# Kernel tuning notes

Hardware: AMD Instinct MI355X
Metric: run time of the kernel (lower is better)

The kernel has to match this reference:

```python
import jax, jax.numpy as jnp
import numpy as np

D = 1024
H = 16
HD = D // H  # 64
FF = 4 * D
EPS = 1e-5

def _layernorm(x, g, b):
    mu = jnp.mean(x, axis=-1, keepdims=True)
    var = jnp.mean((x - mu) ** 2, axis=-1, keepdims=True)
    return (x - mu) * jax.lax.rsqrt(var + EPS) * g + b

def _apply_rotary(x, cos, sin):
    # x: [B,H,T,HD]; cos/sin: [T,HD//2] broadcast over B,H
    d = x.shape[-1] // 2
    x1, x2 = x[..., :d], x[..., d:]
    return jnp.concatenate([x1 * cos - x2 * sin, x2 * cos + x1 * sin], axis=-1)

def setup_inputs() -> dict:
    key = jax.random.key(0)
    ks = jax.random.split(key, 12)
    B, T = 4, 2048
    s = 0.02
    return {
        "x": jax.random.normal(ks[0], (B, T, D), jnp.float32),
        "rope_cos": jax.random.uniform(ks[1], (T, HD // 2), jnp.float32),
        "rope_sin": jax.random.uniform(ks[2], (T, HD // 2), jnp.float32),
        "ln1_g": jnp.ones((D,), jnp.float32),
        "ln1_b": jnp.zeros((D,), jnp.float32),
        "Wqkv": jax.random.normal(ks[3], (D, 3 * D), jnp.float32) * s,
        "bqkv": jnp.zeros((3 * D,), jnp.float32),
        "Wo": jax.random.normal(ks[4], (D, D), jnp.float32) * s,
        "bo": jnp.zeros((D,), jnp.float32),
        "ln2_g": jnp.ones((D,), jnp.float32),
        "ln2_b": jnp.zeros((D,), jnp.float32),
        "W1": jax.random.normal(ks[5], (D, FF), jnp.float32) * s,
        "b1": jnp.zeros((FF,), jnp.float32),
        "W2": jax.random.normal(ks[6], (FF, D), jnp.float32) * s,
        "b2": jnp.zeros((D,), jnp.float32),
    }

def reference(x, rope_cos, rope_sin, ln1_g, ln1_b, Wqkv, bqkv, Wo, bo, ln2_g, ln2_b, W1, b1, W2, b2):
    B, T, _ = x.shape
    h = _layernorm(x, ln1_g, ln1_b)
    qkv = (h @ Wqkv + bqkv).reshape(B, T, 3, H, HD)
    qkv = jnp.transpose(qkv, (2, 0, 3, 1, 4))  # [3,B,H,T,HD]
    q, k, v = qkv[0], qkv[1], qkv[2]
    q = _apply_rotary(q, rope_cos, rope_sin)
    k = _apply_rotary(k, rope_cos, rope_sin)
    scale = 1.0 / jnp.sqrt(jnp.float32(HD))
    scores = jnp.einsum('bhqd,bhkd->bhqk', q, k) * scale
    probs = jax.nn.softmax(scores, axis=-1)
    attn = jnp.einsum('bhqk,bhkd->bhqd', probs, v)
    attn = jnp.transpose(attn, (0, 2, 1, 3)).reshape(B, T, D)
    x = x + attn @ Wo + bo
    h2 = _layernorm(x, ln2_g, ln2_b)
    mlp = jax.nn.gelu(h2 @ W1 + b1, approximate=False) @ W2 + b2
    return x + mlp
```

## Files before the change

### kernel.cpp

```cpp
#include <hip/hip_runtime.h>
#include <hip/hip_bf16.h>
#include <math.h>

typedef __bf16 bf16x8 __attribute__((ext_vector_type(8)));
typedef float f32x4 __attribute__((ext_vector_type(4)));
typedef float f32x16 __attribute__((ext_vector_type(16)));
typedef unsigned short u16x8 __attribute__((ext_vector_type(8)));
typedef unsigned short u16x4 __attribute__((ext_vector_type(4)));
typedef unsigned int u32x4 __attribute__((ext_vector_type(4)));

#define DEV __device__ __forceinline__

DEV unsigned short f2bf(float f) { __bf16 h = (__bf16)f; return __builtin_bit_cast(unsigned short, h); }
DEV float bf2f(unsigned short u) { __bf16 h = __builtin_bit_cast(__bf16, u); return (float)h; }
DEV unsigned int pk2(float a, float b) {
  return (unsigned int)f2bf(a) | ((unsigned int)f2bf(b) << 16);
}

DEV void async_cp16(const void* g, void* l) {
  __builtin_amdgcn_global_load_lds((const __attribute__((address_space(1))) void*)g,
                                   (__attribute__((address_space(3))) void*)l, 16, 0, 0);
}

#define PHASE_BAR()  do { __builtin_amdgcn_s_barrier(); __builtin_amdgcn_sched_barrier(0); } while (0)
#define WAIT_LGKM0() do { asm volatile("s_waitcnt lgkmcnt(0)" ::: "memory"); __builtin_amdgcn_sched_barrier(0); } while (0)
#define WAIT_VM(n)   do { asm volatile("s_waitcnt vmcnt(" #n ")" ::: "memory"); __builtin_amdgcn_sched_barrier(0); } while (0)

__global__ __launch_bounds__(256) void ln_kernel(const float* __restrict__ in,
    const float* __restrict__ g, const float* __restrict__ b,
    unsigned short* __restrict__ out)
{
  const int row = blockIdx.x;
  const int tid = threadIdx.x;
  const float4 v = ((const float4*)(in + (size_t)row * 1024))[tid];
  float s  = v.x + v.y + v.z + v.w;
  float sq = v.x*v.x + v.y*v.y + v.z*v.z + v.w*v.w;
  for (int m = 1; m < 64; m <<= 1) { s += __shfl_xor(s, m); sq += __shfl_xor(sq, m); }
  __shared__ float red[8];
  const int wave = tid >> 6;
  if ((tid & 63) == 0) { red[wave] = s; red[4 + wave] = sq; }
  __syncthreads();
  s  = red[0] + red[1] + red[2] + red[3];
  sq = red[4] + red[5] + red[6] + red[7];
  const float mu = s * (1.0f / 1024.0f);
  const float var = sq * (1.0f / 1024.0f) - mu * mu;
  const float rs = rsqrtf(var + 1e-5f);
  const float4 gv = ((const float4*)g)[tid];
  const float4 bv = ((const float4*)b)[tid];
  u16x4 o;
  o[0] = f2bf((v.x - mu) * rs * gv.x + bv.x);
  o[1] = f2bf((v.y - mu) * rs * gv.y + bv.y);
  o[2] = f2bf((v.z - mu) * rs * gv.z + bv.z);
  o[3] = f2bf((v.w - mu) * rs * gv.w + bv.w);
  *(u16x4*)(out + (size_t)row * 1024 + tid * 4) = o;
}

__global__ __launch_bounds__(256) void wtrans_kernel(const float* __restrict__ in,
    unsigned short* __restrict__ out, int K, int N)
{
  __shared__ float tile[32][33];
  const int n0 = blockIdx.x * 32, k0 = blockIdx.y * 32;
  const int r = threadIdx.x >> 5, c = threadIdx.x & 31;
  for (int p = 0; p < 4; ++p)
    tile[r + p * 8][c] = in[(size_t)(k0 + r + p * 8) * N + n0 + c];
  __syncthreads();
  for (int p = 0; p < 4; ++p)
    out[(size_t)(n0 + r + p * 8) * K + k0 + c] = f2bf(tile[c][r + p * 8]);
}

enum { EPI_QKV = 0, EPI_ATTNO = 1, EPI_GELU = 2, EPI_FINAL = 3 };

template <int EPI>
__global__ __launch_bounds__(256, 3) void gemm_bt(
    const unsigned short* __restrict__ A,
    const unsigned short* __restrict__ Bt,
    const float* __restrict__ bias,
    const float* __restrict__ resid,
    void* __restrict__ out,
    int M, int N, int K,
    const float* __restrict__ rc, const float* __restrict__ rsn,
    unsigned short* __restrict__ vout)
{
  __shared__ unsigned short lA[8192] __attribute__((aligned(16)));
  __shared__ unsigned short lB[8192] __attribute__((aligned(16)));
  const int tid = threadIdx.x;
  const int lane = tid & 63, wave = tid >> 6;
  const int l15 = lane & 15, quad = lane >> 4;
  const int bm = blockIdx.x * 128, bn = blockIdx.y * 128;
  const int wm = (wave & 1) * 64, wn = (wave >> 1) * 64;

  const unsigned short* ga[4]; const unsigned short* gb[4];
  unsigned short* la_dst[4]; unsigned short* lb_dst[4];
  for (int it = 0; it < 4; ++it) {
    const int s = it * 256 + tid;
    const int row = s >> 3;
    const int ch = (s & 7) ^ (row & 7);
    ga[it] = A  + (size_t)(bm + row) * K + ch * 8;
    gb[it] = Bt + (size_t)(bn + row) * K + ch * 8;
    const int base = (it * 256 + wave * 64) * 8;
    la_dst[it] = lA + base;
    lb_dst[it] = lB + base;
  }
  int offA[2][4], offB[2][4];
  for (int ks = 0; ks < 2; ++ks)
    for (int i = 0; i < 4; ++i) {
      int row = wm + i * 16 + l15;
      offA[ks][i] = (row * 8 + ((ks * 4 + quad) ^ (row & 7))) * 8;
      row = wn + i * 16 + l15;
      offB[ks][i] = (row * 8 + ((ks * 4 + quad) ^ (row & 7))) * 8;
    }

  f32x4 acc[4][4];
  for (int i = 0; i < 4; ++i)
    for (int j = 0; j < 4; ++j)
      acc[i][j] = f32x4{0.f, 0.f, 0.f, 0.f};

  for (int k0 = 0; k0 < K; k0 += 64) {
    for (int it = 0; it < 4; ++it) async_cp16(ga[it], la_dst[it]);
    for (int it = 0; it < 4; ++it) async_cp16(gb[it], lb_dst[it]);
    for (int it = 0; it < 4; ++it) { ga[it] += 64; gb[it] += 64; }
    __syncthreads();
    for (int ks = 0; ks < 2; ++ks) {
      bf16x8 af[4], bfr[4];
      for (int i = 0; i < 4; ++i) af[i]  = *(const bf16x8*)(lA + offA[ks][i]);
      for (int j = 0; j < 4; ++j) bfr[j] = *(const bf16x8*)(lB + offB[ks][j]);
      for (int i = 0; i < 4; ++i)
        for (int j = 0; j < 4; ++j)
          acc[i][j] = __builtin_amdgcn_mfma_f32_16x16x32_bf16(af[i], bfr[j], acc[i][j], 0, 0, 0);
    }
    __syncthreads();
  }

  float bvals[4];
  for (int j = 0; j < 4; ++j) bvals[j] = bias[bn + wn + j * 16 + l15];

  for (int i = 0; i < 4; ++i) {
    for (int r = 0; r < 4; ++r) {
      const size_t row = bm + wm + i * 16 + quad * 4 + r;
      for (int j = 0; j < 4; ++j) {
        const size_t col = bn + wn + j * 16 + l15;
        const float v = acc[i][j][r] + bvals[j];
        const size_t idx = row * (size_t)N + col;
        if constexpr (EPI == EPI_ATTNO) {
          ((float*)out)[idx] = resid[idx] + v;
        } else if constexpr (EPI == EPI_GELU) {
          const float gl = 0.5f * v * (1.0f + erff(v * 0.70710678118f));
          ((unsigned short*)out)[idx] = f2bf(gl);
        } else {
          ((float*)out)[idx] = resid[idx] + v;
        }
      }
    }
  }
}

template <int EPI>
__global__ __launch_bounds__(512, 1) void gemm256(
    const unsigned short* __restrict__ A,
    const unsigned short* __restrict__ Bt,
    const float* __restrict__ bias,
    void* __restrict__ out,
    int M, int N, int K,
    const float* __restrict__ rc, const float* __restrict__ rsn,
    unsigned short* __restrict__ vout)
{
  __shared__ unsigned short lA[2][16384] __attribute__((aligned(16)));
  __shared__ unsigned short lB[2][16384] __attribute__((aligned(16)));
  const int tid = threadIdx.x;
  const int lane = tid & 63, wave = tid >> 6;
  const int l15 = lane & 15, quad = lane >> 4;
  const int bm = blockIdx.x * 256, bn = blockIdx.y * 256;
  const int wr = wave >> 2, wc = wave & 3;
  const int wm = wr * 128, wn = wc * 64;

  const unsigned short* gA[4]; const unsigned short* gB[4];
  {
    const int r0 = tid >> 3;
    const int ch = (tid & 7) ^ (r0 & 7);
    for (int it = 0; it < 4; ++it) {
      gA[it] = A  + (size_t)(bm + it * 64 + r0) * K + ch * 8;
      gB[it] = Bt + (size_t)(bn + it * 64 + r0) * K + ch * 8;
    }
  }
  const int ldsbase = wave * 512;

  const int swz = l15 & 7;
  const int oA0 = (wm + l15) * 64 + ((quad) ^ swz) * 8;
  const int oA1 = (wm + l15) * 64 + ((4 + quad) ^ swz) * 8;
  const int oB0 = (wn + l15) * 64 + ((quad) ^ swz) * 8;
  const int oB1 = (wn + l15) * 64 + ((4 + quad) ^ swz) * 8;

  f32x4 acc[8][4];
  for (int i = 0; i < 8; ++i)
    for (int j = 0; j < 4; ++j)
      acc[i][j] = f32x4{0.f, 0.f, 0.f, 0.f};

  const int NT = K >> 6;

  async_cp16(gB[0], lB[0] + 0    + ldsbase);
  async_cp16(gB[1], lB[0] + 4096 + ldsbase);
  async_cp16(gB[2], lB[0] + 8192 + ldsbase);
  async_cp16(gB[3], lB[0] + 12288 + ldsbase);
  async_cp16(gA[0], lA[0] + 0    + ldsbase);
  async_cp16(gA[2], lA[0] + 8192 + ldsbase);
  async_cp16(gA[1], lA[0] + 4096 + ldsbase);
  async_cp16(gA[3], lA[0] + 12288 + ldsbase);
  for (int it = 0; it < 4; ++it) { gA[it] += 64; gB[it] += 64; }
  WAIT_VM(2);
  PHASE_BAR();

  for (int t = 0; t < NT; ++t) {
    const unsigned short* lAc = lA[t & 1];
    const unsigned short* lBc = lB[t & 1];
    unsigned short* lAn = lA[(t & 1) ^ 1];
    unsigned short* lBn = lB[(t & 1) ^ 1];
    const bool pf = (t + 1 < NT);
    bf16x8 af[4], bfr[4];

    for (int i = 0; i < 4; ++i) af[i]  = *(const bf16x8*)(lAc + oA0 + i * 1024);
    for (int j = 0; j < 4; ++j) bfr[j] = *(const bf16x8*)(lBc + oB0 + j * 1024);
    if (pf) { async_cp16(gB[0], lBn + 0 + ldsbase); async_cp16(gB[1], lBn + 4096 + ldsbase); }
    PHASE_BAR(); WAIT_LGKM0();
    __builtin_amdgcn_s_setprio(1);
    for (int i = 0; i < 4; ++i)
      for (int j = 0; j < 4; ++j)
        acc[i][j] = __builtin_amdgcn_mfma_f32_16x16x32_bf16(af[i], bfr[j], acc[i][j], 0, 0, 0);
    __builtin_amdgcn_s_setprio(0);
    if (pf) { WAIT_VM(2); } else { WAIT_VM(0); }
    PHASE_BAR();

    for (int i = 0; i < 4; ++i) af[i] = *(const bf16x8*)(lAc + oA0 + (4 + i) * 1024);
    if (pf) { async_cp16(gB[2], lBn + 8192 + ldsbase); async_cp16(gB[3], lBn + 12288 + ldsbase); }
    PHASE_BAR(); WAIT_LGKM0();
    __builtin_amdgcn_s_setprio(1);
    for (int i = 0; i < 4; ++i)
      for (int j = 0; j < 4; ++j)
        acc[4 + i][j] = __builtin_amdgcn_mfma_f32_16x16x32_bf16(af[i], bfr[j], acc[4 + i][j], 0, 0, 0);
    __builtin_amdgcn_s_setprio(0);
    PHASE_BAR();

    for (int i = 0; i < 4; ++i) af[i]  = *(const bf16x8*)(lAc + oA1 + i * 1024);
    for (int j = 0; j < 4; ++j) bfr[j] = *(const bf16x8*)(lBc + oB1 + j * 1024);
    if (pf) { async_cp16(gA[0], lAn + 0 + ldsbase); async_cp16(gA[2], lAn + 8192 + ldsbase); }
    PHASE_BAR(); WAIT_LGKM0();
    __builtin_amdgcn_s_setprio(1);
    for (int i = 0; i < 4; ++i)
      for (int j = 0; j < 4; ++j)
        acc[i][j] = __builtin_amdgcn_mfma_f32_16x16x32_bf16(af[i], bfr[j], acc[i][j], 0, 0, 0);
    __builtin_amdgcn_s_setprio(0);
    PHASE_BAR();

    for (int i = 0; i < 4; ++i) af[i] = *(const bf16x8*)(lAc + oA1 + (4 + i) * 1024);
    if (pf) { async_cp16(gA[1], lAn + 4096 + ldsbase); async_cp16(gA[3], lAn + 12288 + ldsbase); }
    PHASE_BAR(); WAIT_LGKM0();
    __builtin_amdgcn_s_setprio(1);
    for (int i = 0; i < 4; ++i)
      for (int j = 0; j < 4; ++j)
        acc[4 + i][j] = __builtin_amdgcn_mfma_f32_16x16x32_bf16(af[i], bfr[j], acc[4 + i][j], 0, 0, 0);
    __builtin_amdgcn_s_setprio(0);
    if (pf) { WAIT_VM(2); }
    PHASE_BAR();

    if (pf) for (int it = 0; it < 4; ++it) { gA[it] += 64; gB[it] += 64; }
  }

  float bvals[4];
  for (int j = 0; j < 4; ++j) bvals[j] = bias[bn + wn + j * 16 + l15];

  if constexpr (EPI == EPI_QKV) {
    const int cn = bn + wn;
    const int sec = cn >> 10;
    if (sec == 2) {
      const int b = bm >> 11;
      const int hh = (cn & 1023) >> 6;
      for (int i = 0; i < 8; ++i) {
        const int t0 = (bm + wm + i * 16 + quad * 4) & 2047;
        for (int j = 0; j < 4; ++j) {
          const int d = j * 16 + l15;
          u16x4 o;
          for (int r = 0; r < 4; ++r) o[r] = f2bf(acc[i][j][r] + bvals[j]);
          *(u16x4*)(vout + ((size_t)((b * 16 + hh) * 64 + d)) * 2048 + t0) = o;
        }
      }
    } else {
      const float qscale = (sec == 0) ? 0.18033688f : 1.0f;
      unsigned short* qkvout = (unsigned short*)out;
      for (int i = 0; i < 8; ++i) {
        for (int r = 0; r < 4; ++r) {
          const int row = bm + wm + i * 16 + quad * 4 + r;
          const int tt = row & 2047;
          for (int j = 0; j < 2; ++j) {
            const int d = j * 16 + l15;
            const float v1 = acc[i][j][r] + bvals[j];
            const float v2 = acc[i][j + 2][r] + bvals[j + 2];
            const float c = rc[tt * 32 + d], s = rsn[tt * 32 + d];
            const float o1 = (v1 * c - v2 * s) * qscale;
            const float o2 = (v2 * c + v1 * s) * qscale;
            const size_t base = (size_t)row * 3072 + cn + d;
            qkvout[base] = f2bf(o1);
            qkvout[base + 32] = f2bf(o2);
          }
        }
      }
    }
  } else {
    unsigned short* o = (unsigned short*)out;
    for (int i = 0; i < 8; ++i)
      for (int r = 0; r < 4; ++r) {
        const size_t row = bm + wm + i * 16 + quad * 4 + r;
        for (int j = 0; j < 4; ++j) {
          const size_t col = bn + wn + j * 16 + l15;
          const float v = acc[i][j][r] + bvals[j];
          const float gl = 0.5f * v * (1.0f + erff(v * 0.70710678118f));
          o[row * (size_t)N + col] = f2bf(gl);
        }
      }
  }
}

__global__ __launch_bounds__(256, 4) void attn_kernel(
    const unsigned short* __restrict__ qkv,
    const unsigned short* __restrict__ vt,
    unsigned short* __restrict__ outb)
{
  __shared__ unsigned short Ks[2][4096] __attribute__((aligned(16)));
  __shared__ unsigned short Vs[2][4096] __attribute__((aligned(16)));
  __shared__ float Sred[128];

  const int tid = threadIdx.x;
  const int lane = tid & 63, wave = tid >> 6;
  const int l31 = lane & 31, hl = lane >> 5;
  const int bh = blockIdx.y, b = bh >> 4, h = bh & 15;
  const int q0 = blockIdx.x * 128;
  const int qsub = wave * 32;

  bf16x8 qf[4];
  {
    const unsigned short* qp = qkv + (size_t)(b * 2048 + q0 + qsub + l31) * 3072 + h * 64 + hl * 8;
    for (int kc = 0; kc < 4; ++kc) qf[kc] = *(const bf16x8*)(qp + kc * 16);
  }

  const int s0 = wave * 128 + lane, s1 = s0 + 64;
  const int r0 = s0 >> 3, c0 = (lane & 7) ^ (r0 & 7);
  const int r1 = s1 >> 3, c1 = (lane & 7) ^ (r1 & 7);
  const unsigned short* kbase = qkv + (size_t)(b * 2048) * 3072 + 1024 + h * 64;
  const unsigned short* ks0 = kbase + (size_t)r0 * 3072 + c0 * 8;
  const unsigned short* ks1 = kbase + (size_t)r1 * 3072 + c1 * 8;
  const unsigned short* vbase = vt + (size_t)bh * 64 * 2048;
  const unsigned short* vs0 = vbase + (size_t)r0 * 2048 + c0 * 8;
  const unsigned short* vs1 = vbase + (size_t)r1 * 2048 + c1 * 8;
  unsigned short* kd[2] = { Ks[0] + wave * 1024, Ks[1] + wave * 1024 };
  unsigned short* vd[2] = { Vs[0] + wave * 1024, Vs[1] + wave * 1024 };

  int offK[2][4], offV[2][4];
  for (int g = 0; g < 2; ++g)
    for (int kc = 0; kc < 4; ++kc) {
      const int rk = g * 32 + l31;
      offK[g][kc] = (rk * 8 + ((2 * kc + hl) ^ (rk & 7))) * 8;
    }
  for (int dn = 0; dn < 2; ++dn)
    for (int t = 0; t < 4; ++t) {
      const int rv = dn * 32 + l31;
      offV[dn][t] = (rv * 8 + ((2 * t + hl) ^ (rv & 7))) * 8;
    }

  f32x16 accO[2];
  for (int dn = 0; dn < 2; ++dn)
    for (int i = 0; i < 16; ++i) accO[dn][i] = 0.f;
  float rsum = 0.f;

  async_cp16(ks0, kd[0]);
  async_cp16(ks1, kd[0] + 512);
  async_cp16(vs0, vd[0]);
  async_cp16(vs1, vd[0] + 512);

  for (int kt = 0; kt < 32; ++kt) {
    const int cur = kt & 1, nxt = cur ^ 1;
    __syncthreads();
    if (kt < 31) {
      const size_t ko = (size_t)(kt + 1) * 64 * 3072;
      const int vo = (kt + 1) * 64;
      async_cp16(ks0 + ko, kd[nxt]);
      async_cp16(ks1 + ko, kd[nxt] + 512);
      async_cp16(vs0 + vo, vd[nxt]);
      async_cp16(vs1 + vo, vd[nxt] + 512);
    }
    for (int g = 0; g < 2; ++g) {
      f32x16 accS;
      for (int i = 0; i < 16; ++i) accS[i] = 0.f;
      for (int kc = 0; kc < 4; ++kc) {
        const bf16x8 kf = *(const bf16x8*)(Ks[cur] + offK[g][kc]);
        accS = __builtin_amdgcn_mfma_f32_32x32x16_bf16(kf, qf[kc], accS, 0, 0, 0);
      }
      float p[16];
      for (int i = 0; i < 16; ++i) {
        p[i] = __builtin_amdgcn_exp2f(accS[i]);
        rsum += p[i];
      }
      for (int c = 0; c < 2; ++c) {
        const unsigned int xlo0 = pk2(p[8 * c + 0], p[8 * c + 1]);
        const unsigned int xlo1 = pk2(p[8 * c + 2], p[8 * c + 3]);
        const unsigned int xhi0 = pk2(p[8 * c + 4], p[8 * c + 5]);
        const unsigned int xhi1 = pk2(p[8 * c + 6], p[8 * c + 7]);
        const auto sw0 = __builtin_amdgcn_permlane32_swap(xlo0, xhi0, false, false);
        const auto sw1 = __builtin_amdgcn_permlane32_swap(xlo1, xhi1, false, false);
        u32x4 w;
        w[0] = sw0[0];
        w[1] = sw1[0];
        w[2] = sw0[1];
        w[3] = sw1[1];
        const bf16x8 pf = __builtin_bit_cast(bf16x8, w);
        const int t = 2 * g + c;
        for (int dn = 0; dn < 2; ++dn) {
          const bf16x8 vf = *(const bf16x8*)(Vs[cur] + offV[dn][t]);
          accO[dn] = __builtin_amdgcn_mfma_f32_32x32x16_bf16(pf, vf, accO[dn], 0, 0, 0);
        }
      }
    }
  }

  {
    const float rs2 = rsum + __shfl_xor(rsum, 32);
    if (hl == 0) Sred[qsub + l31] = rs2;
  }
  __syncthreads();
  for (int reg = 0; reg < 16; ++reg) {
    const int rq = qsub + (reg & 3) + 8 * (reg >> 2) + 4 * hl;
    const float inv = 1.0f / Sred[rq];
    const size_t row = (size_t)(b * 2048 + q0 + rq);
    for (int dn = 0; dn < 2; ++dn)
      outb[row * 1024 + h * 64 + dn * 32 + l31] = f2bf(accO[dn][reg] * inv);
  }
}

extern "C" void kernel_launch(void* const* d_in, const int* in_sizes, int n_in,
                              void* d_out, int out_size, void* d_ws, size_t ws_size,
                              hipStream_t stream)
{
  const float* x        = (const float*)d_in[0];
  const float* rope_cos = (const float*)d_in[1];
  const float* rope_sin = (const float*)d_in[2];
  const float* ln1_g    = (const float*)d_in[3];
  const float* ln1_b    = (const float*)d_in[4];
  const float* Wqkv     = (const float*)d_in[5];
  const float* bqkv     = (const float*)d_in[6];
  const float* Wo       = (const float*)d_in[7];
  const float* bo       = (const float*)d_in[8];
  const float* ln2_g    = (const float*)d_in[9];
  const float* ln2_b    = (const float*)d_in[10];
  const float* W1       = (const float*)d_in[11];
  const float* b1       = (const float*)d_in[12];
  const float* W2       = (const float*)d_in[13];
  const float* b2       = (const float*)d_in[14];
  float* outp = (float*)d_out;

  char* ws = (char*)d_ws;
  size_t off = 0;
  auto alloc = [&](size_t bytes) -> void* {
    void* p = ws + off;
    off += (bytes + 255) & ~(size_t)255;
    return p;
  };
  unsigned short* h1    = (unsigned short*)alloc(8192ull * 1024 * 2);
  unsigned short* wqkvT = (unsigned short*)alloc(3072ull * 1024 * 2);
  unsigned short* woT   = (unsigned short*)alloc(1024ull * 1024 * 2);
  unsigned short* w1T   = (unsigned short*)alloc(4096ull * 1024 * 2);
  unsigned short* w2T   = (unsigned short*)alloc(1024ull * 4096 * 2);
  unsigned short* qkv   = (unsigned short*)alloc(8192ull * 3072 * 2);
  unsigned short* vtb   = (unsigned short*)alloc(64ull * 64 * 2048 * 2);
  unsigned short* h2    = (unsigned short*)alloc(8192ull * 1024 * 2);
  unsigned short* ffb   = (unsigned short*)alloc(8192ull * 4096 * 2);

  wtrans_kernel<<<dim3(96, 32), 256, 0, stream>>>(Wqkv, wqkvT, 1024, 3072);
  wtrans_kernel<<<dim3(32, 32), 256, 0, stream>>>(Wo, woT, 1024, 1024);
  wtrans_kernel<<<dim3(128, 32), 256, 0, stream>>>(W1, w1T, 1024, 4096);
  wtrans_kernel<<<dim3(32, 128), 256, 0, stream>>>(W2, w2T, 4096, 1024);

  ln_kernel<<<8192, 256, 0, stream>>>(x, ln1_g, ln1_b, h1);
  gemm256<EPI_QKV><<<dim3(32, 12), 512, 0, stream>>>(h1, wqkvT, bqkv, qkv,
                                                     8192, 3072, 1024, rope_cos, rope_sin, vtb);
  attn_kernel<<<dim3(16, 64), 256, 0, stream>>>(qkv, vtb, h1);
  gemm_bt<EPI_ATTNO><<<dim3(64, 8), 256, 0, stream>>>(h1, woT, bo, x, d_out,
                                                      8192, 1024, 1024, nullptr, nullptr, nullptr);
  ln_kernel<<<8192, 256, 0, stream>>>(outp, ln2_g, ln2_b, h2);
  gemm256<EPI_GELU><<<dim3(32, 16), 512, 0, stream>>>(h2, w1T, b1, ffb,
                                                      8192, 4096, 1024, nullptr, nullptr, nullptr);
  gemm_bt<EPI_FINAL><<<dim3(64, 8), 256, 0, stream>>>(ffb, w2T, b2, outp, d_out,
                                                      8192, 1024, 4096, nullptr, nullptr, nullptr);
}
```

Before: 605.6 us.

## Pin GEMM accumulators to AGPRs and target two waves per EU

Replaces the MFMA builtin with inline asm that keeps the accumulators in AGPRs. It also sets waves_per_eu(2,2) so two 512-thread blocks can share a CU, and recomputes global load addresses from a single lane offset instead of keeping eight pointers live. The aim is to lower VGPR pressure so occupancy can double and LDS latency is better hidden. The inline asm hides dependencies from the compiler's scheduler, which is why manual s_nops are added after the loop to cover the MFMA result hazard. The LDS use of 128KB per block may still limit residency to one block per CU.

```diff
diff --git a/kernel.cpp b/kernel.cpp
--- a/kernel.cpp
+++ b/kernel.cpp
@@ -20,6 +20,11 @@
 DEV void async_cp16(const void* g, void* l) {
   __builtin_amdgcn_global_load_lds((const __attribute__((address_space(1))) void*)g,
                                    (__attribute__((address_space(3))) void*)l, 16, 0, 0);
+}
+
+DEV void mfma_agpr(f32x4& c, bf16x8 a, bf16x8 b) {
+  asm volatile("v_mfma_f32_16x16x32_bf16 %0, %1, %2, %0"
+               : "+a"(c) : "v"(a), "v"(b));
 }
 
 #define PHASE_BAR()  do { __builtin_amdgcn_s_barrier(); __builtin_amdgcn_sched_barrier(0); } while (0)
@@ -155,7 +160,9 @@
 }
 
 template <int EPI>
-__global__ __launch_bounds__(512, 1) void gemm256(
+__global__ __launch_bounds__(512)
+__attribute__((amdgpu_waves_per_eu(2, 2)))
+void gemm256(
     const unsigned short* __restrict__ A,
     const unsigned short* __restrict__ Bt,
     const float* __restrict__ bias,
@@ -173,15 +180,9 @@
   const int wr = wave >> 2, wc = wave & 3;
   const int wm = wr * 128, wn = wc * 64;
 
-  const unsigned short* gA[4]; const unsigned short* gB[4];
-  {
-    const int r0 = tid >> 3;
-    const int ch = (tid & 7) ^ (r0 & 7);
-    for (int it = 0; it < 4; ++it) {
-      gA[it] = A  + (size_t)(bm + it * 64 + r0) * K + ch * 8;
-      gB[it] = Bt + (size_t)(bn + it * 64 + r0) * K + ch * 8;
-    }
-  }
+  const int r0 = tid >> 3;
+  const int ch = (tid & 7) ^ (r0 & 7);
+  const size_t laneOff = (size_t)r0 * K + ch * 8;
   const int ldsbase = wave * 512;
 
   const int swz = l15 & 7;
@@ -197,15 +198,16 @@
 
   const int NT = K >> 6;
 
-  async_cp16(gB[0], lB[0] + 0    + ldsbase);
-  async_cp16(gB[1], lB[0] + 4096 + ldsbase);
-  async_cp16(gB[2], lB[0] + 8192 + ldsbase);
-  async_cp16(gB[3], lB[0] + 12288 + ldsbase);
-  async_cp16(gA[0], lA[0] + 0    + ldsbase);
-  async_cp16(gA[2], lA[0] + 8192 + ldsbase);
-  async_cp16(gA[1], lA[0] + 4096 + ldsbase);
-  async_cp16(gA[3], lA[0] + 12288 + ldsbase);
-  for (int it = 0; it < 4; ++it) { gA[it] += 64; gB[it] += 64; }
+  auto stA = [&](int it, int k0, unsigned short* dst) {
+    async_cp16(A + (size_t)(bm + it * 64) * K + k0 + laneOff, dst + it * 4096 + ldsbase);
+  };
+  auto stB = [&](int it, int k0, unsigned short* dst) {
+    async_cp16(Bt + (size_t)(bn + it * 64) * K + k0 + laneOff, dst + it * 4096 + ldsbase);
+  };
+
+  stB(0, 0, lB[0]); stB(1, 0, lB[0]); stB(2, 0, lB[0]); stB(3, 0, lB[0]);
+  stA(0, 0, lA[0]); stA(2, 0, lA[0]);
+  stA(1, 0, lA[0]); stA(3, 0, lA[0]);
   WAIT_VM(2);
   PHASE_BAR();
 
@@ -215,54 +217,55 @@
     unsigned short* lAn = lA[(t & 1) ^ 1];
     unsigned short* lBn = lB[(t & 1) ^ 1];
     const bool pf = (t + 1 < NT);
+    const int kn = (t + 1) * 64;
     bf16x8 af[4], bfr[4];
 
     for (int i = 0; i < 4; ++i) af[i]  = *(const bf16x8*)(lAc + oA0 + i * 1024);
     for (int j = 0; j < 4; ++j) bfr[j] = *(const bf16x8*)(lBc + oB0 + j * 1024);
-    if (pf) { async_cp16(gB[0], lBn + 0 + ldsbase); async_cp16(gB[1], lBn + 4096 + ldsbase); }
+    if (pf) { stB(0, kn, lBn); stB(1, kn, lBn); }
     PHASE_BAR(); WAIT_LGKM0();
     __builtin_amdgcn_s_setprio(1);
     for (int i = 0; i < 4; ++i)
       for (int j = 0; j < 4; ++j)
-        acc[i][j] = __builtin_amdgcn_mfma_f32_16x16x32_bf16(af[i], bfr[j], acc[i][j], 0, 0, 0);
+        mfma_agpr(acc[i][j], af[i], bfr[j]);
     __builtin_amdgcn_s_setprio(0);
     if (pf) { WAIT_VM(2); } else { WAIT_VM(0); }
     PHASE_BAR();
 
     for (int i = 0; i < 4; ++i) af[i] = *(const bf16x8*)(lAc + oA0 + (4 + i) * 1024);
-    if (pf) { async_cp16(gB[2], lBn + 8192 + ldsbase); async_cp16(gB[3], lBn + 12288 + ldsbase); }
+    if (pf) { stB(2, kn, lBn); stB(3, kn, lBn); }
     PHASE_BAR(); WAIT_LGKM0();
     __builtin_amdgcn_s_setprio(1);
     for (int i = 0; i < 4; ++i)
       for (int j = 0; j < 4; ++j)
-        acc[4 + i][j] = __builtin_amdgcn_mfma_f32_16x16x32_bf16(af[i], bfr[j], acc[4 + i][j], 0, 0, 0);
+        mfma_agpr(acc[4 + i][j], af[i], bfr[j]);
     __builtin_amdgcn_s_setprio(0);
     PHASE_BAR();
 
     for (int i = 0; i < 4; ++i) af[i]  = *(const bf16x8*)(lAc + oA1 + i * 1024);
     for (int j = 0; j < 4; ++j) bfr[j] = *(const bf16x8*)(lBc + oB1 + j * 1024);
-    if (pf) { async_cp16(gA[0], lAn + 0 + ldsbase); async_cp16(gA[2], lAn + 8192 + ldsbase); }
+    if (pf) { stA(0, kn, lAn); stA(2, kn, lAn); }
     PHASE_BAR(); WAIT_LGKM0();
     __builtin_amdgcn_s_setprio(1);
     for (int i = 0; i < 4; ++i)
       for (int j = 0; j < 4; ++j)
-        acc[i][j] = __builtin_amdgcn_mfma_f32_16x16x32_bf16(af[i], bfr[j], acc[i][j], 0, 0, 0);
+        mfma_agpr(acc[i][j], af[i], bfr[j]);
     __builtin_amdgcn_s_setprio(0);
     PHASE_BAR();
 
     for (int i = 0; i < 4; ++i) af[i] = *(const bf16x8*)(lAc + oA1 + (4 + i) * 1024);
-    if (pf) { async_cp16(gA[1], lAn + 4096 + ldsbase); async_cp16(gA[3], lAn + 12288 + ldsbase); }
+    if (pf) { stA(1, kn, lAn); stA(3, kn, lAn); }
     PHASE_BAR(); WAIT_LGKM0();
     __builtin_amdgcn_s_setprio(1);
     for (int i = 0; i < 4; ++i)
       for (int j = 0; j < 4; ++j)
-        acc[4 + i][j] = __builtin_amdgcn_mfma_f32_16x16x32_bf16(af[i], bfr[j], acc[4 + i][j], 0, 0, 0);
+        mfma_agpr(acc[4 + i][j], af[i], bfr[j]);
     __builtin_amdgcn_s_setprio(0);
     if (pf) { WAIT_VM(2); }
     PHASE_BAR();
-
-    if (pf) for (int it = 0; it < 4; ++it) { gA[it] += 64; gB[it] += 64; }
-  }
+  }
+
+  asm volatile("s_nop 7\n\ts_nop 7\n\ts_nop 7" :::);
 
   float bvals[4];
   for (int j = 0; j < 4; ++j) bvals[j] = bias[bn + wn + j * 16 + l15];
```

New measurement: 628.3 us. +3.7%, slower.
